# Performance work log

Hardware: AMD Instinct MI355X
Metric: run time of the kernel (lower is better)

The kernel has to match this reference:

```python
import jax, jax.numpy as jnp
import numpy as np

B, C, H, W = 4, 256, 48, 48
KD, NH, AR = 32, 8, 4
D = AR * KD            # 128, value dim per head
NHKD = NH * KD         # 256
DH = NH * D            # 1024
EPS = 1e-5


def _bn(y, g, b):
    # BN with fresh running stats (mean=0, var=1): y*g/sqrt(1+eps)+b, over channel dim
    s = g / jnp.sqrt(jnp.float32(1.0) + EPS)
    return y * s[None, :, None] + b[None, :, None]


def setup_inputs() -> dict:
    key = jax.random.key(0)
    ks = jax.random.split(key, 13)
    w = lambda k, sh: jax.random.normal(k, sh, jnp.float32) * 0.05
    g = lambda k, sh: 1.0 + jax.random.normal(k, sh, jnp.float32) * 0.05
    return {
        "x": jax.random.normal(ks[0], (B, C, H, W), jnp.float32),
        "wq": w(ks[1], (NHKD, C)), "gq": g(ks[2], (NHKD,)), "bq": w(ks[3], (NHKD,)),
        "wk": w(ks[4], (NHKD, C)), "gk": g(ks[5], (NHKD,)), "bk": w(ks[6], (NHKD,)),
        "wv": w(ks[7], (DH, C)),   "gv": g(ks[8], (DH,)),   "bv": w(ks[9], (DH,)),
        "wp": w(ks[10], (C, DH)),  "gp": g(ks[11], (C,)),   "bp": w(ks[12], (C,)),
    }


def reference(x, wq, gq, bq, wk, gk, bk, wv, gv, bv, wp, gp, bp):
    b, c, h, w = x.shape
    n = h * w
    xf = x.reshape(b, c, n)                                   # [B,C,N]
    # 1x1 conv == channel matmul, then BN
    q = _bn(jnp.einsum('oc,bcn->bon', wq, xf), gq, bq).reshape(b, NH, KD, n)
    k = _bn(jnp.einsum('oc,bcn->bon', wk, xf), gk, bk).reshape(b, NH, KD, n)
    v = _bn(jnp.einsum('oc,bcn->bon', wv, xf), gv, bv).reshape(b, NH, D, n)
    # NOTE: original forward does NOT apply self.scale
    attn = jax.nn.softmax(jnp.einsum('bhkn,bhkm->bhnm', q, k), axis=-1)  # [B,H,N,N]
    xx = jnp.einsum('bhnm,bhdm->bhdn', attn, v).reshape(b, DH, n)        # [B,DH,N]
    out = _bn(jnp.einsum('oc,bcn->bon', wp, jax.nn.relu(xx)), gp, bp)
    return out.reshape(b, c, h, w)
```

## Files before the change

### kernel.cpp

```cpp
#include <hip/hip_runtime.h>

#define BB 4
#define C 256
#define HW 2304
#define NH 8
#define KD 32
#define D 128
#define DH 1024
#define MQ 256

typedef unsigned short bf16u;
typedef __attribute__((ext_vector_type(8))) short short8;
typedef __attribute__((ext_vector_type(4))) short bfx4;
typedef __attribute__((ext_vector_type(4))) float f32x4;
typedef __attribute__((ext_vector_type(4))) unsigned ux4;
typedef __attribute__((ext_vector_type(2))) unsigned ux2;

union U8 { ux4 u; short8 s; };
union V8 { short8 s; bfx4 h[2]; };

__device__ __forceinline__ bf16u f2b(float f) {
    unsigned u = __float_as_uint(f);
    return (bf16u)((u + 0x7fffu + ((u >> 16) & 1u)) >> 16);
}
__device__ __forceinline__ unsigned pkb(float a, float b) {
    return __builtin_amdgcn_perm(__float_as_uint(b) + 0x8000u,
                                 __float_as_uint(a) + 0x8000u, 0x07060302u);
}

__device__ __forceinline__ void glds16(const bf16u* g, bf16u* l) {
    __builtin_amdgcn_global_load_lds(
        (const __attribute__((address_space(1))) unsigned int*)g,
        (__attribute__((address_space(3))) unsigned int*)l,
        16, 0, 0);
}

#define MFMA32 __builtin_amdgcn_mfma_f32_16x16x32_bf16

__global__ __launch_bounds__(256) void prep(
    const float* __restrict__ wq, const float* __restrict__ wk, const float* __restrict__ wv,
    const float* __restrict__ gq, const float* __restrict__ bq,
    const float* __restrict__ gk, const float* __restrict__ bk,
    const float* __restrict__ gv, const float* __restrict__ bv,
    bf16u* __restrict__ WcT, float* __restrict__ biasc)
{
    const float rs = rsqrtf(1.0f + 1e-5f);
    const float L2E = 1.4426950408889634f;
    const int t = threadIdx.x, blk = blockIdx.x;
    if (blk < 192) {
        const int idx = (blk*256 + t) * 8;
        const int row = idx >> 8;
        const int k   = idx & 255;
        const float* src; float sc;
        if (row < 256)      { src = wq + idx;            sc = gq[row]*rs*L2E; }
        else if (row < 512) { src = wk + (idx - 65536);  sc = gk[row-256]*rs; }
        else                { src = wv + (idx - 131072); sc = gv[row-512]*rs; }
        float4 a = *(const float4*)(src);
        float4 c = *(const float4*)(src + 4);
        ux4 v;
        v.x = pkb(a.x*sc, a.y*sc); v.y = pkb(a.z*sc, a.w*sc);
        v.z = pkb(c.x*sc, c.y*sc); v.w = pkb(c.z*sc, c.w*sc);
        const size_t dst = (size_t)((row>>7)*8 + (k>>5))*4096
                         + (size_t)((row&127)*4 + ((k&31)>>3))*8;
        *(ux4*)(WcT + dst) = v;
    } else {
        #pragma unroll
        for (int kk = 0; kk < 6; ++kk) {
            const int r = kk*256 + t;
            float v;
            if (r < 256)      v = bq[r] * L2E;
            else if (r < 512) v = bk[r - 256];
            else              v = bv[r - 512];
            biasc[r] = v;
        }
    }
}

__global__ __launch_bounds__(256) void xtrans(const float* __restrict__ x,
                                              bf16u* __restrict__ xT)
{
    const int c0 = blockIdx.x * 64, n0 = blockIdx.y * 64, b = blockIdx.z;
    const int t = threadIdx.x;
    __shared__ float tile[64][68];

    const float* xb = x + (size_t)b * C * HW;
    #pragma unroll
    for (int rr = 0; rr < 4; ++rr) {
        const int cl = rr*16 + (t >> 4);
        float4 v = *(const float4*)(xb + (size_t)(c0 + cl) * HW + n0 + (t & 15)*4);
        tile[cl][(t&15)*4+0] = v.x; tile[cl][(t&15)*4+1] = v.y;
        tile[cl][(t&15)*4+2] = v.z; tile[cl][(t&15)*4+3] = v.w;
    }
    __syncthreads();
    const int nl = t >> 2, ch = t & 3;
    short8 v0, v1;
    #pragma unroll
    for (int kk = 0; kk < 8; ++kk) v0[kk] = (short)f2b(tile[ch*16+kk][nl]);
    #pragma unroll
    for (int kk = 0; kk < 8; ++kk) v1[kk] = (short)f2b(tile[ch*16+8+kk][nl]);
    bf16u* dst = xT + ((size_t)b*HW + n0 + nl) * C + c0 + ch*16;
    *(short8*)(dst)     = v0;
    *(short8*)(dst + 8) = v1;
}

__global__ __launch_bounds__(256, 3) void qkv_gemm(
    const bf16u* __restrict__ WcT, const float* __restrict__ biasc,
    const bf16u* __restrict__ xT,
    bf16u* __restrict__ qT, bf16u* __restrict__ kT, bf16u* __restrict__ vO)
{
    const int mt = blockIdx.x, ntb = blockIdx.y, b = blockIdx.z;
    const int r0 = mt * 128, c0 = ntb * 128;
    const int t = threadIdx.x, w = t >> 6, l = t & 63;
    const int l15 = l & 15, q = l >> 4;
    const int wr = w >> 1, wc = w & 1;

    __shared__ bf16u smem[24576];

    const bf16u* xb = xT + (size_t)b * HW * C;

    const int sA0 = w*128 + l, sA1 = w*128 + 64 + l;
    const bf16u* gA0 = WcT + (size_t)mt*32768 + (size_t)sA0*8;
    const bf16u* gA1 = WcT + (size_t)mt*32768 + (size_t)sA1*8;
    const bf16u* gB0 = xb + (size_t)(c0 + (sA0>>2)) * C + (sA0&3)*8;
    const bf16u* gB1 = xb + (size_t)(c0 + (sA1>>2)) * C + (sA1&3)*8;

    f32x4 acc[4][4];
    #pragma unroll
    for (int i = 0; i < 4; ++i)
        #pragma unroll
        for (int j = 0; j < 4; ++j) { acc[i][j][0]=0.f; acc[i][j][1]=0.f; acc[i][j][2]=0.f; acc[i][j][3]=0.f; }

    auto stage = [&](int it2, int bb) {
        bf16u* As = smem + bb*4096;
        bf16u* Bs = smem + 12288 + bb*4096;
        glds16(gA0 + it2*4096, As + sA0*8);
        glds16(gA1 + it2*4096, As + sA1*8);
        glds16(gB0 + it2*32,   Bs + sA0*8);
        glds16(gB1 + it2*32,   Bs + sA1*8);
    };

    const bool isV = (r0 >= 512);
    stage(0, 0); stage(1, 1);
    for (int it = 0; it < 8; ++it) {
        __syncthreads();
        if (it + 2 < 8) stage(it + 2, (it + 2) % 3);
        const bf16u* A = smem + (it % 3) * 4096;
        const bf16u* B = smem + 12288 + (it % 3) * 4096;
        short8 af[4], bf[4];
        #pragma unroll
        for (int i = 0; i < 4; ++i) af[i] = *(const short8*)(A + (wr*64 + i*16 + l15)*32 + q*8);
        #pragma unroll
        for (int j = 0; j < 4; ++j) bf[j] = *(const short8*)(B + (wc*64 + j*16 + l15)*32 + q*8);
        if (!isV) {
            #pragma unroll
            for (int i = 0; i < 4; ++i)
                #pragma unroll
                for (int j = 0; j < 4; ++j)
                    acc[i][j] = MFMA32(af[i], bf[j], acc[i][j], 0, 0, 0);
        } else {
            #pragma unroll
            for (int i = 0; i < 4; ++i)
                #pragma unroll
                for (int j = 0; j < 4; ++j)
                    acc[i][j] = MFMA32(bf[j], af[i], acc[i][j], 0, 0, 0);
        }
    }

    __syncthreads();
    bf16u* Od = smem + w * 4096;

    if (!isV) {
        float bC[4][4];
        #pragma unroll
        for (int i = 0; i < 4; ++i)
            #pragma unroll
            for (int r = 0; r < 4; ++r)
                bC[i][r] = biasc[r0 + wr*64 + i*16 + q*4 + r];
        #pragma unroll
        for (int i = 0; i < 4; ++i)
            #pragma unroll
            for (int j = 0; j < 4; ++j) {
                float y0 = acc[i][j][0] + bC[i][0];
                float y1 = acc[i][j][1] + bC[i][1];
                float y2 = acc[i][j][2] + bC[i][2];
                float y3 = acc[i][j][3] + bC[i][3];
                ux2 pk; pk.x = pkb(y0, y1); pk.y = pkb(y2, y3);
                const int row = j*16 + l15;
                const int ch  = (i*2 + (q >> 1)) ^ (l15 & 7);
                *(ux2*)(Od + row*64 + ch*8 + (q & 1)*4) = pk;
            }
        bf16u* dst = (r0 < 256) ? qT : kT;
        const int n = c0 + wc*64 + l;
        #pragma unroll
        for (int c = 0; c < 8; ++c) {
            short8 v = *(const short8*)(Od + l*64 + ((c ^ (l & 7)) * 8));
            const int ocg = (r0 & 255) + wr*64 + c*8;
            const int h = ocg >> 5, kd0 = ocg & 31;
            *(short8*)(dst + ((size_t)(b*NH + h) * HW + n) * KD + kd0) = v;
        }
    } else {
        float bC[4];
        #pragma unroll
        for (int i = 0; i < 4; ++i)
            bC[i] = biasc[r0 + wr*64 + i*16 + l15];
        #pragma unroll
        for (int i = 0; i < 4; ++i)
            #pragma unroll
            for (int j = 0; j < 4; ++j) {
                float y0 = acc[i][j][0] + bC[i];
                float y1 = acc[i][j][1] + bC[i];
                float y2 = acc[i][j][2] + bC[i];
                float y3 = acc[i][j][3] + bC[i];
                ux2 pk; pk.x = pkb(y0, y1); pk.y = pkb(y2, y3);
                const int row = i*16 + l15;
                const int ch  = (j*2 + (q >> 1)) ^ (l15 & 7);
                *(ux2*)(Od + row*64 + ch*8 + (q & 1)*4) = pk;
            }
        bf16u* dst = vO + (size_t)b * DH * HW;
        const int d = (r0 - 512) + wr*64 + l;
        #pragma unroll
        for (int c = 0; c < 8; ++c) {
            V8 v; v.s = *(const short8*)(Od + l*64 + ((c ^ (l & 7)) * 8));
            const int kh = c >> 2;
            const int g0 = (2*c) & 7;
            const int pos0 = kh*32 + (g0 & 3)*8 + (g0 >> 2)*4;
            const int g1 = g0 + 1;
            const int pos1 = kh*32 + (g1 & 3)*8 + (g1 >> 2)*4;
            bf16u* dr = dst + (size_t)d * HW + c0 + wc*64;
            *(bfx4*)(dr + pos0) = v.h[0];
            *(bfx4*)(dr + pos1) = v.h[1];
        }
    }
}

__global__ __launch_bounds__(256, 4) void attn_mfma(
    const bf16u* __restrict__ qT, const bf16u* __restrict__ kT,
    const bf16u* __restrict__ vg, bf16u* __restrict__ xg)
{
    const int nt = blockIdx.x, h = blockIdx.y, b = blockIdx.z;
    const int n0 = nt * 64;
    const int t = threadIdx.x;
    const int w = t >> 6, l = t & 63, l15 = l & 15, q = l >> 4;

    const bf16u* qTh = qT + (size_t)(b*NH + h) * HW * KD;
    const bf16u* kTh = kT + (size_t)(b*NH + h) * HW * KD;
    const bf16u* vh  = vg + ((size_t)b*DH + (size_t)h*D) * HW;

    __shared__ bf16u smem[16384];

    short8 qf = *(const short8*)(qTh + (size_t)(n0 + w*16 + l15) * KD + q*8);

    f32x4 o[8];
    #pragma unroll
    for (int d = 0; d < 8; ++d) { o[d][0]=0.f; o[d][1]=0.f; o[d][2]=0.f; o[d][3]=0.f; }
    float psum = 0.f;
    const f32x4 zero = {0.f, 0.f, 0.f, 0.f};

    auto stageV = [&](int m0, int bb) {
        bf16u* Vs = smem + bb*8192;
        #pragma unroll
        for (int j = 0; j < 4; ++j) {
            const int s = (w*4 + j)*64 + l;
            const int d = s >> 3, c = s & 7, cg = c ^ (d & 7);
            glds16(vh + (size_t)d*HW + m0 + cg*8, Vs + (w*4 + j)*512);
        }
    };

    short8 kfc[4];
    #pragma unroll
    for (int kt = 0; kt < 4; ++kt)
        kfc[kt] = *(const short8*)(kTh + (size_t)(kt*16 + l15) * KD + q*8);
    stageV(0, 0);

    for (int mt = 0; mt < 36; ++mt) {
        __syncthreads();
        if (mt < 35) stageV((mt+1)*64, (mt+1)&1);
        const bf16u* Vs = smem + (mt&1)*8192;

        short8 kfn[4];
        if (mt < 35) {
            #pragma unroll
            for (int kt = 0; kt < 4; ++kt)
                kfn[kt] = *(const short8*)(kTh + (size_t)((mt+1)*64 + kt*16 + l15) * KD + q*8);
        }

        f32x4 st[4];
        #pragma unroll
        for (int kt = 0; kt < 4; ++kt)
            st[kt] = MFMA32(kfc[kt], qf, zero, 0, 0, 0);

        unsigned dA[4], dB[4];
        #pragma unroll
        for (int kt = 0; kt < 4; ++kt) {
            float p0 = __builtin_amdgcn_exp2f(st[kt][0]);
            float p1 = __builtin_amdgcn_exp2f(st[kt][1]);
            float p2 = __builtin_amdgcn_exp2f(st[kt][2]);
            float p3 = __builtin_amdgcn_exp2f(st[kt][3]);
            psum += (p0 + p1) + (p2 + p3);
            dA[kt] = pkb(p0, p1); dB[kt] = pkb(p2, p3);
        }

        #pragma unroll
        for (int kh = 0; kh < 2; ++kh) {
            U8 u;
            u.u[0] = dA[kh*2];   u.u[1] = dB[kh*2];
            u.u[2] = dA[kh*2+1]; u.u[3] = dB[kh*2+1];
            #pragma unroll
            for (int dt = 0; dt < 8; ++dt) {
                const int d = dt*16 + l15;
                short8 vf = *(const short8*)(Vs + d*64 + (((kh*4 + q) ^ (d & 7)) * 8));
                o[dt] = MFMA32(u.s, vf, o[dt], 0, 0, 0);
            }
        }

        if (mt < 35) {
            #pragma unroll
            for (int kt = 0; kt < 4; ++kt) kfc[kt] = kfn[kt];
        }
    }

    psum += __shfl_xor(psum, 16); psum += __shfl_xor(psum, 32);
    float inv[4];
    #pragma unroll
    for (int r = 0; r < 4; ++r)
        inv[r] = 1.0f / __shfl(psum, q*4 + r);
    __syncthreads();
    bf16u* Od = smem + w * 2176;
    #pragma unroll
    for (int dt = 0; dt < 8; ++dt)
        #pragma unroll
        for (int r = 0; r < 4; ++r) {
            float v = fmaxf(o[dt][r] * inv[r], 0.f);
            Od[(q*4 + r)*136 + dt*16 + l15] = f2b(v);
        }
    bf16u* xb = xg + ((size_t)b*HW + n0 + w*16) * DH + h*D;
    const int row = l >> 2, c = l & 3;
    #pragma unroll
    for (int kk = 0; kk < 4; ++kk)
        *(short8*)(xb + (size_t)row*DH + c*32 + kk*8) =
            *(const short8*)(Od + row*136 + c*32 + kk*8);
}

__global__ __launch_bounds__(256) void prep2(
    const float* __restrict__ wp, const float* __restrict__ gp,
    bf16u* __restrict__ WpT)
{
    const float rs = rsqrtf(1.0f + 1e-5f);
    const int item = blockIdx.x*256 + threadIdx.x;
    const int row = item >> 7;
    const int k   = (item & 127) * 8;
    const float sc = gp[row] * rs;
    const float* src = wp + (size_t)row*DH + k;
    float4 a = *(const float4*)(src);
    float4 c = *(const float4*)(src + 4);
    ux4 v;
    v.x = pkb(a.x*sc, a.y*sc); v.y = pkb(a.z*sc, a.w*sc);
    v.z = pkb(c.x*sc, c.y*sc); v.w = pkb(c.z*sc, c.w*sc);
    const size_t dst = (size_t)((row>>6)*16 + (k>>6))*4096
                     + (size_t)((row&63)*8 + ((k&63)>>3))*8;
    *(ux4*)(WpT + dst) = v;
}

__global__ __launch_bounds__(256, 3) void out_gemm(
    const bf16u* __restrict__ WpT, const float* __restrict__ bp,
    const bf16u* __restrict__ xx, float* __restrict__ out)
{
    const int mt = blockIdx.x, ntb = blockIdx.y, b = blockIdx.z;
    const int r0 = mt * 64, c0 = ntb * 64;
    const int t = threadIdx.x, w = t >> 6, l = t & 63;
    const int l15 = l & 15, q = l >> 4;
    const int wr = w >> 1, wc = w & 1;

    __shared__ bf16u smem[24576];

    const bf16u* xb = xx + (size_t)b * HW * DH;

    const int sA0 = t, sA1 = 256 + t;
    const bf16u* gA0 = WpT + (size_t)mt*65536 + (size_t)sA0*8;
    const bf16u* gA1 = WpT + (size_t)mt*65536 + (size_t)sA1*8;
    const int sB0 = w*128 + l, sB1 = w*128 + 64 + l;
    const bf16u* gB0 = xb + (size_t)(c0 + (sB0>>3)) * DH + (sB0&7)*8;
    const bf16u* gB1 = xb + (size_t)(c0 + (sB1>>3)) * DH + (sB1&7)*8;

    f32x4 acc[2][2];
    #pragma unroll
    for (int i = 0; i < 2; ++i)
        #pragma unroll
        for (int j = 0; j < 2; ++j) { acc[i][j][0]=0.f; acc[i][j][1]=0.f; acc[i][j][2]=0.f; acc[i][j][3]=0.f; }

    auto stage = [&](int it2, int bb) {
        bf16u* As = smem + bb*4096;
        bf16u* Bs = smem + 12288 + bb*4096;
        glds16(gA0 + it2*4096, As + sA0*8);
        glds16(gA1 + it2*4096, As + sA1*8);
        glds16(gB0 + it2*64,   Bs + sB0*8);
        glds16(gB1 + it2*64,   Bs + sB1*8);
    };

    stage(0, 0); stage(1, 1);
    for (int it = 0; it < 16; ++it) {
        __syncthreads();
        if (it + 2 < 16) stage(it + 2, (it + 2) % 3);
        const bf16u* A = smem + (it % 3) * 4096;
        const bf16u* B = smem + 12288 + (it % 3) * 4096;
        #pragma unroll
        for (int kk = 0; kk < 2; ++kk) {
            short8 af[2], bf[2];
            #pragma unroll
            for (int i = 0; i < 2; ++i) af[i] = *(const short8*)(A + (wr*32 + i*16 + l15)*64 + kk*32 + q*8);
            #pragma unroll
            for (int j = 0; j < 2; ++j) bf[j] = *(const short8*)(B + (wc*32 + j*16 + l15)*64 + kk*32 + q*8);
            #pragma unroll
            for (int i = 0; i < 2; ++i)
                #pragma unroll
                for (int j = 0; j < 2; ++j)
                    acc[i][j] = MFMA32(af[i], bf[j], acc[i][j], 0, 0, 0);
        }
    }

    #pragma unroll
    for (int i = 0; i < 2; ++i)
        #pragma unroll
        for (int r = 0; r < 4; ++r) {
            const int oc = r0 + wr*32 + i*16 + q*4 + r;
            const float bi = bp[oc];
            #pragma unroll
            for (int j = 0; j < 2; ++j) {
                const int n = c0 + wc*32 + j*16 + l15;
                out[((size_t)b*C + oc)*HW + n] = acc[i][j][r] + bi;
            }
        }
}

extern "C" void kernel_launch(void* const* d_in, const int* in_sizes, int n_in,
                              void* d_out, int out_size, void* d_ws, size_t ws_size,
                              hipStream_t stream) {
    const float* x  = (const float*)d_in[0];
    const float* wq = (const float*)d_in[1];
    const float* gq = (const float*)d_in[2];
    const float* bq = (const float*)d_in[3];
    const float* wk = (const float*)d_in[4];
    const float* gk = (const float*)d_in[5];
    const float* bk = (const float*)d_in[6];
    const float* wv = (const float*)d_in[7];
    const float* gv = (const float*)d_in[8];
    const float* bv = (const float*)d_in[9];
    const float* wp = (const float*)d_in[10];
    const float* gp = (const float*)d_in[11];
    const float* bp = (const float*)d_in[12];
    float* out = (float*)d_out;

    bf16u* qw = (bf16u*)d_ws;
    bf16u* kw = qw + (size_t)BB * MQ * HW;
    bf16u* vw = kw + (size_t)BB * MQ * HW;
    bf16u* xw = vw + (size_t)BB * DH * HW;
    bf16u* xTb = xw;
    bf16u* WcT = xw + (size_t)BB * MQ * HW;
    float* biasc = (float*)(WcT + 393216);
    bf16u* WpT = qw;

    hipLaunchKernelGGL(prep, dim3(193), dim3(256), 0, stream,
                       wq, wk, wv, gq, bq, gk, bk, gv, bv, WcT, biasc);
    hipLaunchKernelGGL(xtrans, dim3(4, 36, BB), dim3(256), 0, stream, x, xTb);
    hipLaunchKernelGGL(qkv_gemm, dim3(12, 18, BB), dim3(256), 0, stream,
                       WcT, biasc, xTb, qw, kw, vw);
    hipLaunchKernelGGL(attn_mfma, dim3(36, NH, BB), dim3(256), 0, stream,
                       qw, kw, vw, xw);
    hipLaunchKernelGGL(prep2, dim3(128), dim3(256), 0, stream, wp, gp, WpT);
    hipLaunchKernelGGL(out_gemm, dim3(4, 36, BB), dim3(256), 0, stream,
                       WpT, bp, xw, out);
}
```

Measured before the change: 219.5 us.

## Enlarge attention query tile to 128 and split head dim across waves

Each attention block now covers 128 queries instead of 64. Waves are split into two query halves and two halves of the value dimension, so each wave holds 4 query groups times 4 d-tiles of accumulators. Every staged V tile and every K fragment is therefore reused across twice as many queries, which halves K/V traffic per query and the number of blocks. In exchange, QK^T and exp work is duplicated across the two d-half waves, register pressure rises (launch bounds lowered to 2), and the grid drops to 576 blocks.

```diff
diff --git a/kernel.cpp b/kernel.cpp
--- a/kernel.cpp
+++ b/kernel.cpp
@@ -233,27 +233,33 @@
     }
 }
 
-__global__ __launch_bounds__(256, 4) void attn_mfma(
+__global__ __launch_bounds__(256, 2) void attn_mfma(
     const bf16u* __restrict__ qT, const bf16u* __restrict__ kT,
     const bf16u* __restrict__ vg, bf16u* __restrict__ xg)
 {
     const int nt = blockIdx.x, h = blockIdx.y, b = blockIdx.z;
-    const int n0 = nt * 64;
+    const int n0 = nt * 128;
     const int t = threadIdx.x;
     const int w = t >> 6, l = t & 63, l15 = l & 15, q = l >> 4;
+    const int qh = w >> 1, dh = w & 1;
 
     const bf16u* qTh = qT + (size_t)(b*NH + h) * HW * KD;
     const bf16u* kTh = kT + (size_t)(b*NH + h) * HW * KD;
     const bf16u* vh  = vg + ((size_t)b*DH + (size_t)h*D) * HW;
 
-    __shared__ bf16u smem[16384];
-
-    short8 qf = *(const short8*)(qTh + (size_t)(n0 + w*16 + l15) * KD + q*8);
-
-    f32x4 o[8];
-    #pragma unroll
-    for (int d = 0; d < 8; ++d) { o[d][0]=0.f; o[d][1]=0.f; o[d][2]=0.f; o[d][3]=0.f; }
-    float psum = 0.f;
+    __shared__ bf16u smem[18432];
+
+    short8 qf[4];
+    #pragma unroll
+    for (int g = 0; g < 4; ++g)
+        qf[g] = *(const short8*)(qTh + (size_t)(n0 + qh*64 + g*16 + l15) * KD + q*8);
+
+    f32x4 o[4][4];
+    #pragma unroll
+    for (int g = 0; g < 4; ++g)
+        #pragma unroll
+        for (int d = 0; d < 4; ++d) { o[g][d][0]=0.f; o[g][d][1]=0.f; o[g][d][2]=0.f; o[g][d][3]=0.f; }
+    float psum[4] = {0.f, 0.f, 0.f, 0.f};
     const f32x4 zero = {0.f, 0.f, 0.f, 0.f};
 
     auto stageV = [&](int m0, int bb) {
@@ -284,32 +290,39 @@
                 kfn[kt] = *(const short8*)(kTh + (size_t)((mt+1)*64 + kt*16 + l15) * KD + q*8);
         }
 
-        f32x4 st[4];
-        #pragma unroll
-        for (int kt = 0; kt < 4; ++kt)
-            st[kt] = MFMA32(kfc[kt], qf, zero, 0, 0, 0);
-
-        unsigned dA[4], dB[4];
-        #pragma unroll
-        for (int kt = 0; kt < 4; ++kt) {
-            float p0 = __builtin_amdgcn_exp2f(st[kt][0]);
-            float p1 = __builtin_amdgcn_exp2f(st[kt][1]);
-            float p2 = __builtin_amdgcn_exp2f(st[kt][2]);
-            float p3 = __builtin_amdgcn_exp2f(st[kt][3]);
-            psum += (p0 + p1) + (p2 + p3);
-            dA[kt] = pkb(p0, p1); dB[kt] = pkb(p2, p3);
+        unsigned dA[4][4], dB[4][4];
+        #pragma unroll
+        for (int g = 0; g < 4; ++g) {
+            f32x4 st[4];
+            #pragma unroll
+            for (int kt = 0; kt < 4; ++kt)
+                st[kt] = MFMA32(kfc[kt], qf[g], zero, 0, 0, 0);
+            #pragma unroll
+            for (int kt = 0; kt < 4; ++kt) {
+                float p0 = __builtin_amdgcn_exp2f(st[kt][0]);
+                float p1 = __builtin_amdgcn_exp2f(st[kt][1]);
+                float p2 = __builtin_amdgcn_exp2f(st[kt][2]);
+                float p3 = __builtin_amdgcn_exp2f(st[kt][3]);
+                psum[g] += (p0 + p1) + (p2 + p3);
+                dA[g][kt] = pkb(p0, p1); dB[g][kt] = pkb(p2, p3);
+            }
         }
 
         #pragma unroll
         for (int kh = 0; kh < 2; ++kh) {
-            U8 u;
-            u.u[0] = dA[kh*2];   u.u[1] = dB[kh*2];
-            u.u[2] = dA[kh*2+1]; u.u[3] = dB[kh*2+1];
-            #pragma unroll
-            for (int dt = 0; dt < 8; ++dt) {
-                const int d = dt*16 + l15;
+            U8 u[4];
+            #pragma unroll
+            for (int g = 0; g < 4; ++g) {
+                u[g].u[0] = dA[g][kh*2];   u[g].u[1] = dB[g][kh*2];
+                u[g].u[2] = dA[g][kh*2+1]; u[g].u[3] = dB[g][kh*2+1];
+            }
+            #pragma unroll
+            for (int dt = 0; dt < 4; ++dt) {
+                const int d = dh*64 + dt*16 + l15;
                 short8 vf = *(const short8*)(Vs + d*64 + (((kh*4 + q) ^ (d & 7)) * 8));
-                o[dt] = MFMA32(u.s, vf, o[dt], 0, 0, 0);
+                #pragma unroll
+                for (int g = 0; g < 4; ++g)
+                    o[g][dt] = MFMA32(u[g].s, vf, o[g][dt], 0, 0, 0);
             }
         }
 
@@ -319,26 +332,32 @@
         }
     }
 
-    psum += __shfl_xor(psum, 16); psum += __shfl_xor(psum, 32);
-    float inv[4];
-    #pragma unroll
-    for (int r = 0; r < 4; ++r)
-        inv[r] = 1.0f / __shfl(psum, q*4 + r);
+    #pragma unroll
+    for (int g = 0; g < 4; ++g) {
+        psum[g] += __shfl_xor(psum[g], 16);
+        psum[g] += __shfl_xor(psum[g], 32);
+    }
+    float inv[4][4];
+    #pragma unroll
+    for (int g = 0; g < 4; ++g)
+        #pragma unroll
+        for (int r = 0; r < 4; ++r)
+            inv[g][r] = 1.0f / __shfl(psum[g], q*4 + r);
     __syncthreads();
-    bf16u* Od = smem + w * 2176;
-    #pragma unroll
-    for (int dt = 0; dt < 8; ++dt)
-        #pragma unroll
-        for (int r = 0; r < 4; ++r) {
-            float v = fmaxf(o[dt][r] * inv[r], 0.f);
-            Od[(q*4 + r)*136 + dt*16 + l15] = f2b(v);
-        }
-    bf16u* xb = xg + ((size_t)b*HW + n0 + w*16) * DH + h*D;
-    const int row = l >> 2, c = l & 3;
-    #pragma unroll
-    for (int kk = 0; kk < 4; ++kk)
-        *(short8*)(xb + (size_t)row*DH + c*32 + kk*8) =
-            *(const short8*)(Od + row*136 + c*32 + kk*8);
+    bf16u* Od = smem + w * 4608;
+    #pragma unroll
+    for (int g = 0; g < 4; ++g)
+        #pragma unroll
+        for (int dt = 0; dt < 4; ++dt)
+            #pragma unroll
+            for (int r = 0; r < 4; ++r) {
+                float v = fmaxf(o[g][dt][r] * inv[g][r], 0.f);
+                Od[(g*16 + q*4 + r)*72 + dt*16 + l15] = f2b(v);
+            }
+    bf16u* xb = xg + ((size_t)b*HW + n0 + qh*64)*DH + h*D + dh*64;
+    #pragma unroll
+    for (int c = 0; c < 8; ++c)
+        *(short8*)(xb + (size_t)l*DH + c*8) = *(const short8*)(Od + l*72 + c*8);
 }
 
 __global__ __launch_bounds__(256) void prep2(
@@ -464,7 +483,7 @@
     hipLaunchKernelGGL(xtrans, dim3(4, 36, BB), dim3(256), 0, stream, x, xTb);
     hipLaunchKernelGGL(qkv_gemm, dim3(12, 18, BB), dim3(256), 0, stream,
                        WcT, biasc, xTb, qw, kw, vw);
-    hipLaunchKernelGGL(attn_mfma, dim3(36, NH, BB), dim3(256), 0, stream,
+    hipLaunchKernelGGL(attn_mfma, dim3(18, NH, BB), dim3(256), 0, stream,
                        qw, kw, vw, xw);
     hipLaunchKernelGGL(prep2, dim3(128), dim3(256), 0, stream, wp, gp, WpT);
     hipLaunchKernelGGL(out_gemm, dim3(4, 36, BB), dim3(256), 0, stream,
```

Result: slower. 235.7 us (+7.4%).

## Double attention query tile per block and use padded LDS epilogue stores

Applied to the files above, without the earlier changes.

The attention kernel now processes 128 query rows per block, 32 per wave, instead of 64. Each staged K/V tile and each V fragment read from LDS is reused for two query sub-tiles, halving global and LDS traffic per query. This costs more registers, so launch bounds drop to 3 waves per SIMD, and the grid has half as many blocks (576). The QKV GEMM epilogue also switches from an XOR-swizzled LDS layout to a padded stride-72 layout, so global stores are wider and row-contiguous.

```diff
diff --git a/kernel.cpp b/kernel.cpp
--- a/kernel.cpp
+++ b/kernel.cpp
@@ -17,7 +17,6 @@
 typedef __attribute__((ext_vector_type(2))) unsigned ux2;
 
 union U8 { ux4 u; short8 s; };
-union V8 { short8 s; bfx4 h[2]; };
 
 __device__ __forceinline__ bf16u f2b(float f) {
     unsigned u = __float_as_uint(f);
@@ -167,7 +166,7 @@
     }
 
     __syncthreads();
-    bf16u* Od = smem + w * 4096;
+    bf16u* Od = smem + w * 4608;
 
     if (!isV) {
         float bC[4][4];
@@ -185,18 +184,20 @@
                 float y2 = acc[i][j][2] + bC[i][2];
                 float y3 = acc[i][j][3] + bC[i][3];
                 ux2 pk; pk.x = pkb(y0, y1); pk.y = pkb(y2, y3);
-                const int row = j*16 + l15;
-                const int ch  = (i*2 + (q >> 1)) ^ (l15 & 7);
-                *(ux2*)(Od + row*64 + ch*8 + (q & 1)*4) = pk;
+                *(ux2*)(Od + (j*16 + l15)*72 + i*16 + q*4) = pk;
             }
         bf16u* dst = (r0 < 256) ? qT : kT;
-        const int n = c0 + wc*64 + l;
-        #pragma unroll
-        for (int c = 0; c < 8; ++c) {
-            short8 v = *(const short8*)(Od + l*64 + ((c ^ (l & 7)) * 8));
-            const int ocg = (r0 & 255) + wr*64 + c*8;
-            const int h = ocg >> 5, kd0 = ocg & 31;
-            *(short8*)(dst + ((size_t)(b*NH + h) * HW + n) * KD + kd0) = v;
+        #pragma unroll
+        for (int hh = 0; hh < 2; ++hh) {
+            const int h = ((r0 & 255) + wr*64 + hh*32) >> 5;
+            bf16u* dh_ = dst + (size_t)(b*NH + h) * HW * KD;
+            #pragma unroll
+            for (int rg = 0; rg < 4; ++rg) {
+                const int row = rg*16 + (l >> 2);
+                const int n = c0 + wc*64 + row;
+                short8 v = *(const short8*)(Od + row*72 + hh*32 + (l & 3)*8);
+                *(short8*)(dh_ + (size_t)n * KD + (l & 3)*8) = v;
+            }
         }
     } else {
         float bC[4];
@@ -212,33 +213,26 @@
                 float y2 = acc[i][j][2] + bC[i];
                 float y3 = acc[i][j][3] + bC[i];
                 ux2 pk; pk.x = pkb(y0, y1); pk.y = pkb(y2, y3);
-                const int row = i*16 + l15;
-                const int ch  = (j*2 + (q >> 1)) ^ (l15 & 7);
-                *(ux2*)(Od + row*64 + ch*8 + (q & 1)*4) = pk;
+                const int p = (j >> 1)*32 + q*8 + (j & 1)*4;
+                *(ux2*)(Od + (i*16 + l15)*72 + p) = pk;
             }
         bf16u* dst = vO + (size_t)b * DH * HW;
-        const int d = (r0 - 512) + wr*64 + l;
-        #pragma unroll
-        for (int c = 0; c < 8; ++c) {
-            V8 v; v.s = *(const short8*)(Od + l*64 + ((c ^ (l & 7)) * 8));
-            const int kh = c >> 2;
-            const int g0 = (2*c) & 7;
-            const int pos0 = kh*32 + (g0 & 3)*8 + (g0 >> 2)*4;
-            const int g1 = g0 + 1;
-            const int pos1 = kh*32 + (g1 & 3)*8 + (g1 >> 2)*4;
-            bf16u* dr = dst + (size_t)d * HW + c0 + wc*64;
-            *(bfx4*)(dr + pos0) = v.h[0];
-            *(bfx4*)(dr + pos1) = v.h[1];
-        }
-    }
-}
-
-__global__ __launch_bounds__(256, 4) void attn_mfma(
+        #pragma unroll
+        for (int it2 = 0; it2 < 8; ++it2) {
+            const int row = it2*8 + (l >> 3);
+            const int d = (r0 - 512) + wr*64 + row;
+            short8 v = *(const short8*)(Od + row*72 + (l & 7)*8);
+            *(short8*)(dst + (size_t)d * HW + c0 + wc*64 + (l & 7)*8) = v;
+        }
+    }
+}
+
+__global__ __launch_bounds__(256, 3) void attn_mfma(
     const bf16u* __restrict__ qT, const bf16u* __restrict__ kT,
     const bf16u* __restrict__ vg, bf16u* __restrict__ xg)
 {
     const int nt = blockIdx.x, h = blockIdx.y, b = blockIdx.z;
-    const int n0 = nt * 64;
+    const int n0 = nt * 128;
     const int t = threadIdx.x;
     const int w = t >> 6, l = t & 63, l15 = l & 15, q = l >> 4;
 
@@ -246,14 +240,17 @@
     const bf16u* kTh = kT + (size_t)(b*NH + h) * HW * KD;
     const bf16u* vh  = vg + ((size_t)b*DH + (size_t)h*D) * HW;
 
-    __shared__ bf16u smem[16384];
-
-    short8 qf = *(const short8*)(qTh + (size_t)(n0 + w*16 + l15) * KD + q*8);
-
-    f32x4 o[8];
-    #pragma unroll
-    for (int d = 0; d < 8; ++d) { o[d][0]=0.f; o[d][1]=0.f; o[d][2]=0.f; o[d][3]=0.f; }
-    float psum = 0.f;
+    __shared__ bf16u smem[17408];
+
+    short8 qf0 = *(const short8*)(qTh + (size_t)(n0 + w*32 +      l15) * KD + q*8);
+    short8 qf1 = *(const short8*)(qTh + (size_t)(n0 + w*32 + 16 + l15) * KD + q*8);
+
+    f32x4 o[2][8];
+    #pragma unroll
+    for (int a = 0; a < 2; ++a)
+        #pragma unroll
+        for (int d = 0; d < 8; ++d) { o[a][d][0]=0.f; o[a][d][1]=0.f; o[a][d][2]=0.f; o[a][d][3]=0.f; }
+    float psum0 = 0.f, psum1 = 0.f;
     const f32x4 zero = {0.f, 0.f, 0.f, 0.f};
 
     auto stageV = [&](int m0, int bb) {
@@ -266,7 +263,7 @@
         }
     };
 
-    short8 kfc[4];
+    short8 kfc[4], kfn[4];
     #pragma unroll
     for (int kt = 0; kt < 4; ++kt)
         kfc[kt] = *(const short8*)(kTh + (size_t)(kt*16 + l15) * KD + q*8);
@@ -274,42 +271,51 @@
 
     for (int mt = 0; mt < 36; ++mt) {
         __syncthreads();
-        if (mt < 35) stageV((mt+1)*64, (mt+1)&1);
-        const bf16u* Vs = smem + (mt&1)*8192;
-
-        short8 kfn[4];
         if (mt < 35) {
+            stageV((mt+1)*64, (mt+1)&1);
             #pragma unroll
             for (int kt = 0; kt < 4; ++kt)
                 kfn[kt] = *(const short8*)(kTh + (size_t)((mt+1)*64 + kt*16 + l15) * KD + q*8);
         }
-
-        f32x4 st[4];
-        #pragma unroll
-        for (int kt = 0; kt < 4; ++kt)
-            st[kt] = MFMA32(kfc[kt], qf, zero, 0, 0, 0);
-
-        unsigned dA[4], dB[4];
+        const bf16u* Vs = smem + (mt&1)*8192;
+
+        f32x4 st0[4], st1[4];
         #pragma unroll
         for (int kt = 0; kt < 4; ++kt) {
-            float p0 = __builtin_amdgcn_exp2f(st[kt][0]);
-            float p1 = __builtin_amdgcn_exp2f(st[kt][1]);
-            float p2 = __builtin_amdgcn_exp2f(st[kt][2]);
-            float p3 = __builtin_amdgcn_exp2f(st[kt][3]);
-            psum += (p0 + p1) + (p2 + p3);
-            dA[kt] = pkb(p0, p1); dB[kt] = pkb(p2, p3);
+            st0[kt] = MFMA32(kfc[kt], qf0, zero, 0, 0, 0);
+            st1[kt] = MFMA32(kfc[kt], qf1, zero, 0, 0, 0);
+        }
+
+        unsigned dA0[4], dB0[4], dA1[4], dB1[4];
+        #pragma unroll
+        for (int kt = 0; kt < 4; ++kt) {
+            float p0 = __builtin_amdgcn_exp2f(st0[kt][0]);
+            float p1 = __builtin_amdgcn_exp2f(st0[kt][1]);
+            float p2 = __builtin_amdgcn_exp2f(st0[kt][2]);
+            float p3 = __builtin_amdgcn_exp2f(st0[kt][3]);
+            psum0 += (p0 + p1) + (p2 + p3);
+            dA0[kt] = pkb(p0, p1); dB0[kt] = pkb(p2, p3);
+            float r0_ = __builtin_amdgcn_exp2f(st1[kt][0]);
+            float r1_ = __builtin_amdgcn_exp2f(st1[kt][1]);
+            float r2_ = __builtin_amdgcn_exp2f(st1[kt][2]);
+            float r3_ = __builtin_amdgcn_exp2f(st1[kt][3]);
+            psum1 += (r0_ + r1_) + (r2_ + r3_);
+            dA1[kt] = pkb(r0_, r1_); dB1[kt] = pkb(r2_, r3_);
         }
 
         #pragma unroll
         for (int kh = 0; kh < 2; ++kh) {
-            U8 u;
-            u.u[0] = dA[kh*2];   u.u[1] = dB[kh*2];
-            u.u[2] = dA[kh*2+1]; u.u[3] = dB[kh*2+1];
+            U8 u0, u1;
+            u0.u[0] = dA0[kh*2];   u0.u[1] = dB0[kh*2];
+            u0.u[2] = dA0[kh*2+1]; u0.u[3] = dB0[kh*2+1];
+            u1.u[0] = dA1[kh*2];   u1.u[1] = dB1[kh*2];
+            u1.u[2] = dA1[kh*2+1]; u1.u[3] = dB1[kh*2+1];
             #pragma unroll
             for (int dt = 0; dt < 8; ++dt) {
                 const int d = dt*16 + l15;
                 short8 vf = *(const short8*)(Vs + d*64 + (((kh*4 + q) ^ (d & 7)) * 8));
-                o[dt] = MFMA32(u.s, vf, o[dt], 0, 0, 0);
+                o[0][dt] = MFMA32(u0.s, vf, o[0][dt], 0, 0, 0);
+                o[1][dt] = MFMA32(u1.s, vf, o[1][dt], 0, 0, 0);
             }
         }
 
@@ -319,26 +325,36 @@
         }
     }
 
-    psum += __shfl_xor(psum, 16); psum += __shfl_xor(psum, 32);
-    float inv[4];
-    #pragma unroll
-    for (int r = 0; r < 4; ++r)
-        inv[r] = 1.0f / __shfl(psum, q*4 + r);
+    psum0 += __shfl_xor(psum0, 16); psum0 += __shfl_xor(psum0, 32);
+    psum1 += __shfl_xor(psum1, 16); psum1 += __shfl_xor(psum1, 32);
+    float inv0[4], inv1[4];
+    #pragma unroll
+    for (int r = 0; r < 4; ++r) {
+        inv0[r] = 1.0f / __shfl(psum0, q*4 + r);
+        inv1[r] = 1.0f / __shfl(psum1, q*4 + r);
+    }
     __syncthreads();
-    bf16u* Od = smem + w * 2176;
+    bf16u* Od = smem + w * 4352;
     #pragma unroll
     for (int dt = 0; dt < 8; ++dt)
         #pragma unroll
         for (int r = 0; r < 4; ++r) {
-            float v = fmaxf(o[dt][r] * inv[r], 0.f);
-            Od[(q*4 + r)*136 + dt*16 + l15] = f2b(v);
-        }
-    bf16u* xb = xg + ((size_t)b*HW + n0 + w*16) * DH + h*D;
-    const int row = l >> 2, c = l & 3;
-    #pragma unroll
-    for (int kk = 0; kk < 4; ++kk)
-        *(short8*)(xb + (size_t)row*DH + c*32 + kk*8) =
-            *(const short8*)(Od + row*136 + c*32 + kk*8);
+            float v0 = fmaxf(o[0][dt][r] * inv0[r], 0.f);
+            float v1 = fmaxf(o[1][dt][r] * inv1[r], 0.f);
+            Od[(     q*4 + r)*136 + dt*16 + l15] = f2b(v0);
+            Od[(16 + q*4 + r)*136 + dt*16 + l15] = f2b(v1);
+        }
+    bf16u* xb = xg + ((size_t)b*HW + n0 + w*32) * DH + h*D;
+    #pragma unroll
+    for (int g = 0; g < 4; ++g) {
+        const int row = g*8 + (l >> 3);
+        #pragma unroll
+        for (int hf = 0; hf < 2; ++hf) {
+            const int ch = hf*8 + (l & 7);
+            *(short8*)(xb + (size_t)row*DH + ch*8) =
+                *(const short8*)(Od + row*136 + ch*8);
+        }
+    }
 }
 
 __global__ __launch_bounds__(256) void prep2(
@@ -464,7 +480,7 @@
     hipLaunchKernelGGL(xtrans, dim3(4, 36, BB), dim3(256), 0, stream, x, xTb);
     hipLaunchKernelGGL(qkv_gemm, dim3(12, 18, BB), dim3(256), 0, stream,
                        WcT, biasc, xTb, qw, kw, vw);
-    hipLaunchKernelGGL(attn_mfma, dim3(36, NH, BB), dim3(256), 0, stream,
+    hipLaunchKernelGGL(attn_mfma, dim3(18, NH, BB), dim3(256), 0, stream,
                        qw, kw, vw, xw);
     hipLaunchKernelGGL(prep2, dim3(128), dim3(256), 0, stream, wp, gp, WpT);
     hipLaunchKernelGGL(out_gemm, dim3(4, 36, BB), dim3(256), 0, stream,
```

After: 199.2 us. 1.1x faster.
